# Kernel tuning notes

Measured on AMD Instinct MI355X. Metric: run time of the kernel, lower is better.

## Reference

```python
import jax, jax.numpy as jnp
import numpy as np

N_HEADS = 8
N_LEVELS = 1
N_POINTS = 4
D_MODEL = 256
BATCH = 2
H0, W0 = 100, 150
LS = H0 * W0
LQ = 15000


def layer_norm(x, g, b, eps=1e-5):
    m = jnp.mean(x, -1, keepdims=True)
    v = jnp.var(x, -1, keepdims=True)
    return (x - m) * jax.lax.rsqrt(v + eps) * g + b


def bilinear_sample(v, Hl, Wl, loc):
    # v: [N, Hl*Wl, Hh, D] level features; loc in [0,1]: [N, Lq, Hh, P, 2] (x, y)
    Nb, _, Hh, D = v.shape
    Lq, P = loc.shape[1], loc.shape[3]
    x = loc[..., 0] * Wl - 0.5           # align_corners=False grid_sample convention
    y = loc[..., 1] * Hl - 0.5
    x0 = jnp.floor(x); y0 = jnp.floor(y)
    lx = (x - x0).transpose(0, 2, 1, 3)[..., None]   # [N,Hh,Lq,P,1]
    ly = (y - y0).transpose(0, 2, 1, 3)[..., None]
    x0i = x0.astype(jnp.int32); y0i = y0.astype(jnp.int32)
    vh = v.transpose(0, 2, 1, 3)                      # [N,Hh,Hl*Wl,D]

    def gather(xi, yi):
        valid = (xi >= 0) & (xi < Wl) & (yi >= 0) & (yi < Hl)   # zero padding
        idx = jnp.clip(yi, 0, Hl - 1) * Wl + jnp.clip(xi, 0, Wl - 1)
        idxf = idx.transpose(0, 2, 1, 3).reshape(Nb, Hh, Lq * P)
        g = jnp.take_along_axis(vh, idxf[..., None], axis=2).reshape(Nb, Hh, Lq, P, D)
        return g * valid.transpose(0, 2, 1, 3)[..., None]

    g00 = gather(x0i, y0i)
    g10 = gather(x0i + 1, y0i)
    g01 = gather(x0i, y0i + 1)
    g11 = gather(x0i + 1, y0i + 1)
    return (g00 * (1 - lx) * (1 - ly) + g10 * lx * (1 - ly)
            + g01 * (1 - lx) * ly + g11 * lx * ly)   # [N,Hh,Lq,P,D]


def ms_deform_attn(q, reference_points, src, shapes_np, starts_np, padding_mask,
                   W_val, b_val, W_off, b_off, W_attn, b_attn, W_out, b_out):
    Nb, Lq, C = q.shape
    Hh, D, L, P = N_HEADS, C // N_HEADS, N_LEVELS, N_POINTS
    value = src @ W_val + b_val
    value = jnp.where(padding_mask[..., None], 0.0, value).reshape(Nb, -1, Hh, D)
    offsets = (q @ W_off + b_off).reshape(Nb, Lq, Hh, L, P, 2)
    aw = jax.nn.softmax((q @ W_attn + b_attn).reshape(Nb, Lq, Hh, L * P), -1)
    aw = aw.reshape(Nb, Lq, Hh, L, P)
    # offset normalizer is (W, H) per level
    norm = jnp.asarray(shapes_np[:, ::-1].copy(), dtype=q.dtype)   # [L,2]
    loc = reference_points[:, :, None, :, None, :] + offsets / norm[None, None, None, :, None, :]
    out = 0.0
    for l in range(L):
        Hl, Wl = int(shapes_np[l, 0]), int(shapes_np[l, 1])
        s = int(starts_np[l])
        sampled = bilinear_sample(value[:, s:s + Hl * Wl], Hl, Wl, loc[:, :, :, l])
        out = out + jnp.sum(sampled * aw[:, :, :, l].transpose(0, 2, 1, 3)[..., None], axis=3)
    out = out.transpose(0, 2, 1, 3).reshape(Nb, Lq, C)
    return out @ W_out + b_out


def reference(tgt, query_pos, src_pos, tgt_spatial_shapes, reference_points,
              depth_reference_points, src, src_spatial_shapes, frame_start_index,
              src_padding_mask,
              W_dsa, b_dsa, g_nds, b_nds, W_off, b_off, W_attn, b_attn,
              W_val, b_val, W_out, b_out, W_csa, b_csa, g_n1, b_n1,
              W_ff, b_ff, g_n3, b_n3):
    ss = np.asarray(src_spatial_shapes)      # static level shapes
    starts = np.asarray(frame_start_index)
    # depth scale adaptation
    src_a = layer_norm(src @ W_dsa + b_dsa, g_nds, b_nds)
    q = tgt + query_pos
    tgt2 = ms_deform_attn(q, reference_points, src_a, ss, starts, src_padding_mask,
                          W_val, b_val, W_off, b_off, W_attn, b_attn, W_out, b_out)
    tgt2 = tgt2 @ W_csa + b_csa
    t = layer_norm(tgt + tgt2, g_n1, b_n1)
    # FFN: single linear d_model->d_model with exact GELU (per source code)
    ff = jax.nn.gelu(t @ W_ff + b_ff, approximate=False)
    return layer_norm(t + ff, g_n3, b_n3)


def setup_inputs() -> dict:
    key = jax.random.key(0)
    ks = jax.random.split(key, 24)
    C = D_MODEL
    Hh, L, P = N_HEADS, N_LEVELS, N_POINTS

    def lin(k, fin, fout, scale=None):
        s = (1.0 / np.sqrt(fin)) if scale is None else scale
        return (jax.random.normal(k, (fin, fout), jnp.float32) * s).astype(jnp.float32)

    inp = {}
    inp['tgt'] = jax.random.normal(ks[0], (BATCH, LQ, C), jnp.float32)
    inp['query_pos'] = 0.1 * jax.random.normal(ks[1], (BATCH, LQ, C), jnp.float32)
    inp['src_pos'] = 0.1 * jax.random.normal(ks[2], (BATCH, LS, C), jnp.float32)
    inp['tgt_spatial_shapes'] = jnp.array([[H0, W0]], jnp.int32)
    inp['reference_points'] = jax.random.uniform(ks[3], (BATCH, LQ, L, 2), jnp.float32)
    inp['depth_reference_points'] = jax.random.uniform(ks[4], (BATCH, LQ, 1, 2), jnp.float32)
    inp['src'] = jax.random.normal(ks[5], (BATCH, LS, C), jnp.float32)
    inp['src_spatial_shapes'] = jnp.array([[H0, W0]], jnp.int32)
    inp['frame_start_index'] = jnp.array([0], jnp.int32)
    inp['src_padding_mask'] = jnp.zeros((BATCH, LS), jnp.bool_)
    # parameters
    inp['W_dsa'] = lin(ks[6], C, C); inp['b_dsa'] = jnp.zeros((C,), jnp.float32)
    inp['g_nds'] = jnp.ones((C,), jnp.float32); inp['b_nds'] = jnp.zeros((C,), jnp.float32)
    inp['W_off'] = lin(ks[7], C, Hh * L * P * 2, scale=0.01)
    inp['b_off'] = 0.5 * jax.random.normal(ks[8], (Hh * L * P * 2,), jnp.float32)
    inp['W_attn'] = lin(ks[9], C, Hh * L * P)
    inp['b_attn'] = jnp.zeros((Hh * L * P,), jnp.float32)
    inp['W_val'] = lin(ks[10], C, C); inp['b_val'] = jnp.zeros((C,), jnp.float32)
    inp['W_out'] = lin(ks[11], C, C); inp['b_out'] = jnp.zeros((C,), jnp.float32)
    inp['W_csa'] = lin(ks[12], C, C); inp['b_csa'] = jnp.zeros((C,), jnp.float32)
    inp['g_n1'] = jnp.ones((C,), jnp.float32); inp['b_n1'] = jnp.zeros((C,), jnp.float32)
    inp['W_ff'] = lin(ks[13], C, C); inp['b_ff'] = jnp.zeros((C,), jnp.float32)
    inp['g_n3'] = jnp.ones((C,), jnp.float32); inp['b_n3'] = jnp.zeros((C,), jnp.float32)
    return inp
```

## Files before the change

kernel.cpp:

```cpp
#include <hip/hip_runtime.h>
#include <hip/hip_bf16.h>
#include <math.h>

#define LQ   15000
#define LS_  15000
#define NB   2
#define ROWS (NB*LQ)
#define HGT  100
#define WID  150
#define KDIM 256

typedef __attribute__((ext_vector_type(8))) short bf16x8;
typedef __attribute__((ext_vector_type(4))) float f32x4;

enum { EP_BIAS_F32 = 0, EP_LN_BF = 1, EP_MASK_HM = 2, EP_RES_LN_BF = 3, EP_GELU_RES_LN_F32 = 4 };
enum { AM_BF16 = 0, AM_F32 = 1, AM_F32SUM = 2 };

__device__ inline short f2bf(float x) {
    __hip_bfloat16 h = __float2bfloat16(x);
    return *reinterpret_cast<short*>(&h);
}
__device__ inline unsigned pack2bf(float a, float b) {
    return ((unsigned)(unsigned short)f2bf(a)) | (((unsigned)(unsigned short)f2bf(b)) << 16);
}
__device__ inline float bf2f(short s) {
    return __uint_as_float(((unsigned)(unsigned short)s) << 16);
}
__device__ inline float gelu_exact(float x) {
    return 0.5f * x * (1.f + erff(x * 0.70710678118654752440f));
}

template<int NT, int EPI, int AMODE>
__global__ __launch_bounds__(256) void mfma_gemm(
    const void* __restrict__ Ap, const void* __restrict__ Ap2,
    const short* __restrict__ WT,
    const float* __restrict__ bias, void* __restrict__ Out,
    const void* __restrict__ Res, const unsigned char* __restrict__ mask,
    const float* __restrict__ lng, const float* __restrict__ lnb, int M)
{
    constexpr int BN = NT * 16;
    __shared__ short As[64][40];
    __shared__ short Bs[BN][40];
    __shared__ float sbias[BN], sg[BN], sb2[BN];

    const int tid  = threadIdx.x;
    const int bm0  = blockIdx.x * 64;
    const int wave = tid >> 6, lane = tid & 63;
    const int quad = lane >> 4, c = lane & 15;

    if (tid < BN) {
        sbias[tid] = bias ? bias[tid] : 0.f;
        if (EPI == EP_LN_BF || EPI == EP_RES_LN_BF || EPI == EP_GELU_RES_LN_F32) {
            sg[tid] = lng[tid]; sb2[tid] = lnb[tid];
        }
    }

    f32x4 acc[NT];
    #pragma unroll
    for (int t = 0; t < NT; ++t) acc[t] = (f32x4){0.f, 0.f, 0.f, 0.f};

    for (int k0 = 0; k0 < KDIM; k0 += 32) {
        if (AMODE != AM_BF16) {
            const float* A  = (const float*)Ap;
            const float* A2 = (const float*)Ap2;
            #pragma unroll
            for (int it = 0; it < 2; ++it) {
                int f = it * 256 + tid; int m = f >> 3; int ko = (f & 7) * 4;
                int r = bm0 + m; if (r > M - 1) r = M - 1;
                float4 v = *(const float4*)&A[(size_t)r * KDIM + k0 + ko];
                if (AMODE == AM_F32SUM) {
                    float4 w = *(const float4*)&A2[(size_t)r * KDIM + k0 + ko];
                    v.x += w.x; v.y += w.y; v.z += w.z; v.w += w.w;
                }
                int2 p; p.x = pack2bf(v.x, v.y); p.y = pack2bf(v.z, v.w);
                *(int2*)&As[m][ko] = p;
            }
        } else {
            const short* A = (const short*)Ap;
            int m = tid >> 2; int ko = (tid & 3) * 8;
            int r = bm0 + m; if (r > M - 1) r = M - 1;
            *(int4*)&As[m][ko] = *(const int4*)&A[(size_t)r * KDIM + k0 + ko];
        }
        #pragma unroll
        for (int it = 0; it < (BN * 4 + 255) / 256; ++it) {
            int f = it * 256 + tid;
            if (f < BN * 4) {
                int n = f >> 2; int ko = (f & 3) * 8;
                *(int4*)&Bs[n][ko] = *(const int4*)&WT[(size_t)n * KDIM + k0 + ko];
            }
        }
        __syncthreads();
        bf16x8 a = *(const bf16x8*)&As[wave * 16 + c][quad * 8];
        #pragma unroll
        for (int t = 0; t < NT; ++t) {
            bf16x8 b = *(const bf16x8*)&Bs[t * 16 + c][quad * 8];
            acc[t] = __builtin_amdgcn_mfma_f32_16x16x32_bf16(a, b, acc[t], 0, 0, 0);
        }
        __syncthreads();
    }

    const int r0 = bm0 + wave * 16 + quad * 4;
    if constexpr (EPI == EP_BIAS_F32) {
        float* O = (float*)Out;
        #pragma unroll
        for (int reg = 0; reg < 4; ++reg) {
            int r = r0 + reg;
            if (r < M) {
                #pragma unroll
                for (int t = 0; t < NT; ++t)
                    O[(size_t)r * BN + t * 16 + c] = acc[t][reg] + sbias[t * 16 + c];
            }
        }
    } else if constexpr (EPI == EP_MASK_HM) {
        short* O = (short*)Out;
        #pragma unroll
        for (int reg = 0; reg < 4; ++reg) {
            int r = r0 + reg;
            if (r < M) {
                float mz = mask[r] ? 0.f : 1.f;
                int n = (r >= LS_) ? 1 : 0;
                int s = r - n * LS_;
                #pragma unroll
                for (int t = 0; t < NT; ++t) {
                    int col = t * 16 + c;
                    int h = col >> 5, d = col & 31;
                    O[(((size_t)n * 8 + h) * LS_ + s) * 32 + d] =
                        f2bf((acc[t][reg] + sbias[col]) * mz);
                }
            }
        }
    } else {
        #pragma unroll
        for (int reg = 0; reg < 4; ++reg) {
            int r = r0 + reg;
            int rl = (r < M) ? r : (M - 1);
            float s = 0.f, sq = 0.f;
            #pragma unroll
            for (int t = 0; t < NT; ++t) {
                float v = acc[t][reg] + sbias[t * 16 + c];
                if constexpr (EPI == EP_GELU_RES_LN_F32) {
                    v = gelu_exact(v);
                    v += bf2f(((const short*)Res)[(size_t)rl * 256 + t * 16 + c]);
                } else if constexpr (EPI == EP_RES_LN_BF) {
                    v += ((const float*)Res)[(size_t)rl * 256 + t * 16 + c];
                }
                acc[t][reg] = v;
                s += v; sq += v * v;
            }
            #pragma unroll
            for (int o = 1; o < 16; o <<= 1) {
                s  += __shfl_xor(s,  o, 64);
                sq += __shfl_xor(sq, o, 64);
            }
            float mean = s * (1.f / 256.f);
            float var  = sq * (1.f / 256.f) - mean * mean;
            float rs   = rsqrtf(var + 1e-5f);
            if (r < M) {
                #pragma unroll
                for (int t = 0; t < NT; ++t) {
                    float o = (acc[t][reg] - mean) * rs * sg[t * 16 + c] + sb2[t * 16 + c];
                    if constexpr (EPI == EP_GELU_RES_LN_F32)
                        ((float*)Out)[(size_t)r * 256 + t * 16 + c] = o;
                    else
                        ((short*)Out)[(size_t)r * 256 + t * 16 + c] = f2bf(o);
                }
            }
        }
    }
}

__global__ __launch_bounds__(256) void transp_cvt(const float* __restrict__ W, short* __restrict__ WT)
{
    __shared__ float tile[64][65];
    int bx = blockIdx.x * 64, by = blockIdx.y * 64;
    int tid = threadIdx.x;
    #pragma unroll
    for (int it = 0; it < 4; ++it) {
        int f = it * 256 + tid; int i = f >> 4; int j = (f & 15) * 4;
        float4 v = *(const float4*)&W[(size_t)(by + i) * 256 + bx + j];
        tile[i][j] = v.x; tile[i][j + 1] = v.y; tile[i][j + 2] = v.z; tile[i][j + 3] = v.w;
    }
    __syncthreads();
    #pragma unroll
    for (int it = 0; it < 16; ++it) {
        int f = it * 256 + tid; int nl = f >> 6; int kl = f & 63;
        WT[(size_t)(bx + nl) * 256 + by + kl] = f2bf(tile[kl][nl]);
    }
}

__global__ __launch_bounds__(256) void wc_kernel(
    const float* __restrict__ W_out, const float* __restrict__ W_csa, short* __restrict__ WT_c)
{
    int k = blockIdx.x, n = threadIdx.x;
    float s = 0.f;
    for (int j = 0; j < 256; ++j)
        s = fmaf(W_out[(size_t)k * 256 + j], W_csa[(size_t)j * 256 + n], s);
    WT_c[(size_t)n * 256 + k] = f2bf(s);
}

__global__ __launch_bounds__(256) void bias_combine_kernel(
    const float* __restrict__ b_out, const float* __restrict__ W_csa,
    const float* __restrict__ b_csa, float* __restrict__ bc)
{
    int j = threadIdx.x;
    float s = b_csa[j];
    for (int k = 0; k < 256; ++k) s = fmaf(b_out[k], W_csa[(size_t)k * 256 + j], s);
    bc[j] = s;
}

__global__ __launch_bounds__(256) void pack_oa(
    const float* __restrict__ W_off, const float* __restrict__ W_attn,
    const float* __restrict__ b_off, const float* __restrict__ b_attn,
    short* __restrict__ WT_oa, float* __restrict__ b_oa)
{
    int j = blockIdx.x, k = threadIdx.x;
    float v = (j < 64) ? W_off[(size_t)k * 64 + j] : W_attn[(size_t)k * 32 + (j - 64)];
    WT_oa[(size_t)j * 256 + k] = f2bf(v);
    if (k == 0) b_oa[j] = (j < 64) ? b_off[j] : b_attn[j - 64];
}

__global__ __launch_bounds__(256) void deform_sample(
    const short* __restrict__ value,
    const float* __restrict__ S_oa,
    const float* __restrict__ refp,
    short* __restrict__ out)
{
    int grp = blockIdx.x * 32 + (threadIdx.x >> 3);
    int c4  = threadIdx.x & 7;
    int h = grp & 7;
    int r = grp >> 3;
    int n = (r >= LS_) ? 1 : 0;

    const float* row = S_oa + (size_t)r * 96;
    float rx = refp[(size_t)r * 2 + 0], ry = refp[(size_t)r * 2 + 1];
    float4 oA = *(const float4*)&row[h * 8];
    float4 oB = *(const float4*)&row[h * 8 + 4];
    float4 lg = *(const float4*)&row[64 + h * 4];

    float mx = fmaxf(fmaxf(lg.x, lg.y), fmaxf(lg.z, lg.w));
    float e0 = expf(lg.x - mx), e1 = expf(lg.y - mx), e2 = expf(lg.z - mx), e3 = expf(lg.w - mx);
    float inv = 1.f / (e0 + e1 + e2 + e3);
    float aw[4] = {e0 * inv, e1 * inv, e2 * inv, e3 * inv};
    float ox[4] = {oA.x, oA.z, oB.x, oB.z};
    float oy[4] = {oA.y, oA.w, oB.y, oB.w};

    const short* vb = value + (((size_t)n * 8 + h) * LS_) * 32 + c4 * 4;
    float a0 = 0.f, a1 = 0.f, a2 = 0.f, a3 = 0.f;

    #pragma unroll
    for (int p = 0; p < 4; ++p) {
        float x = rx * (float)WID + ox[p] - 0.5f;
        float y = ry * (float)HGT + oy[p] - 0.5f;
        float x0f = floorf(x), y0f = floorf(y);
        float lx = x - x0f, ly = y - y0f;
        int x0 = (int)x0f, y0 = (int)y0f;
        int x1 = x0 + 1, y1 = y0 + 1;
        bool vx0 = (x0 >= 0) & (x0 < WID), vx1 = (x1 >= 0) & (x1 < WID);
        bool vy0 = (y0 >= 0) & (y0 < HGT), vy1 = (y1 >= 0) & (y1 < HGT);
        float w00 = (vx0 & vy0) ? (1.f - lx) * (1.f - ly) * aw[p] : 0.f;
        float w10 = (vx1 & vy0) ? lx * (1.f - ly) * aw[p] : 0.f;
        float w01 = (vx0 & vy1) ? (1.f - lx) * ly * aw[p] : 0.f;
        float w11 = (vx1 & vy1) ? lx * ly * aw[p] : 0.f;
        int xc0 = min(max(x0, 0), WID - 1), xc1 = min(max(x1, 0), WID - 1);
        int yc0 = min(max(y0, 0), HGT - 1), yc1 = min(max(y1, 0), HGT - 1);
        int2 v00 = *(const int2*)&vb[(size_t)(yc0 * WID + xc0) * 32];
        int2 v10 = *(const int2*)&vb[(size_t)(yc0 * WID + xc1) * 32];
        int2 v01 = *(const int2*)&vb[(size_t)(yc1 * WID + xc0) * 32];
        int2 v11 = *(const int2*)&vb[(size_t)(yc1 * WID + xc1) * 32];
        a0 += w00 * __uint_as_float(((unsigned)v00.x) << 16)
            + w10 * __uint_as_float(((unsigned)v10.x) << 16)
            + w01 * __uint_as_float(((unsigned)v01.x) << 16)
            + w11 * __uint_as_float(((unsigned)v11.x) << 16);
        a1 += w00 * __uint_as_float(v00.x & 0xffff0000u)
            + w10 * __uint_as_float(v10.x & 0xffff0000u)
            + w01 * __uint_as_float(v01.x & 0xffff0000u)
            + w11 * __uint_as_float(v11.x & 0xffff0000u);
        a2 += w00 * __uint_as_float(((unsigned)v00.y) << 16)
            + w10 * __uint_as_float(((unsigned)v10.y) << 16)
            + w01 * __uint_as_float(((unsigned)v01.y) << 16)
            + w11 * __uint_as_float(((unsigned)v11.y) << 16);
        a3 += w00 * __uint_as_float(v00.y & 0xffff0000u)
            + w10 * __uint_as_float(v10.y & 0xffff0000u)
            + w01 * __uint_as_float(v01.y & 0xffff0000u)
            + w11 * __uint_as_float(v11.y & 0xffff0000u);
    }
    int2 o;
    o.x = pack2bf(a0, a1);
    o.y = pack2bf(a2, a3);
    *(int2*)&out[(size_t)r * 256 + h * 32 + c4 * 4] = o;
}

extern "C" void kernel_launch(void* const* d_in, const int* in_sizes, int n_in,
                              void* d_out, int out_size, void* d_ws, size_t ws_size,
                              hipStream_t stream)
{
    const float* tgt       = (const float*)d_in[0];
    const float* query_pos = (const float*)d_in[1];
    const float* refp      = (const float*)d_in[4];
    const float* src       = (const float*)d_in[6];
    const unsigned char* mask = (const unsigned char*)d_in[9];
    const float* W_dsa  = (const float*)d_in[10]; const float* b_dsa  = (const float*)d_in[11];
    const float* g_nds  = (const float*)d_in[12]; const float* b_nds  = (const float*)d_in[13];
    const float* W_off  = (const float*)d_in[14]; const float* b_off  = (const float*)d_in[15];
    const float* W_attn = (const float*)d_in[16]; const float* b_attn = (const float*)d_in[17];
    const float* W_val  = (const float*)d_in[18]; const float* b_val  = (const float*)d_in[19];
    const float* W_out  = (const float*)d_in[20]; const float* b_out  = (const float*)d_in[21];
    const float* W_csa  = (const float*)d_in[22]; const float* b_csa  = (const float*)d_in[23];
    const float* g_n1   = (const float*)d_in[24]; const float* b_n1   = (const float*)d_in[25];
    const float* W_ff   = (const float*)d_in[26]; const float* b_ff   = (const float*)d_in[27];
    const float* g_n3   = (const float*)d_in[28]; const float* b_n3   = (const float*)d_in[29];
    float* out = (float*)d_out;

    short* bf0   = (short*)d_ws;
    short* bf1   = bf0 + (size_t)ROWS * 256;
    short* bf2   = bf1 + (size_t)ROWS * 256;
    float* S_oa  = (float*)(bf2 + (size_t)ROWS * 256);
    short* WT_dsa = (short*)(S_oa + (size_t)ROWS * 96);
    short* WT_val = WT_dsa + 65536;
    short* WT_c   = WT_val + 65536;
    short* WT_ff  = WT_c + 65536;
    short* WT_oa  = WT_ff + 65536;
    float* bc     = (float*)(WT_oa + 96 * 256);
    float* b_oa   = bc + 256;

    dim3 blk(256);
    const int GB = (ROWS + 63) / 64;

    transp_cvt<<<dim3(4, 4), blk, 0, stream>>>(W_dsa, WT_dsa);
    transp_cvt<<<dim3(4, 4), blk, 0, stream>>>(W_val, WT_val);
    transp_cvt<<<dim3(4, 4), blk, 0, stream>>>(W_ff,  WT_ff);
    wc_kernel<<<256, blk, 0, stream>>>(W_out, W_csa, WT_c);
    bias_combine_kernel<<<1, blk, 0, stream>>>(b_out, W_csa, b_csa, bc);
    pack_oa<<<96, blk, 0, stream>>>(W_off, W_attn, b_off, b_attn, WT_oa, b_oa);

    mfma_gemm<16, EP_LN_BF, AM_F32><<<GB, blk, 0, stream>>>(
        src, nullptr, WT_dsa, b_dsa, bf0, nullptr, nullptr, g_nds, b_nds, ROWS);
    mfma_gemm<16, EP_MASK_HM, AM_BF16><<<GB, blk, 0, stream>>>(
        bf0, nullptr, WT_val, b_val, bf2, nullptr, mask, nullptr, nullptr, ROWS);
    mfma_gemm<6, EP_BIAS_F32, AM_F32SUM><<<GB, blk, 0, stream>>>(
        tgt, query_pos, WT_oa, b_oa, S_oa, nullptr, nullptr, nullptr, nullptr, ROWS);
    deform_sample<<<ROWS * 8 / 32, blk, 0, stream>>>(bf2, S_oa, refp, bf0);
    mfma_gemm<16, EP_RES_LN_BF, AM_BF16><<<GB, blk, 0, stream>>>(
        bf0, nullptr, WT_c, bc, bf1, tgt, nullptr, g_n1, b_n1, ROWS);
    mfma_gemm<16, EP_GELU_RES_LN_F32, AM_BF16><<<GB, blk, 0, stream>>>(
        bf1, nullptr, WT_ff, b_ff, out, bf1, nullptr, g_n3, b_n3, ROWS);
}
```

Baseline: 347.0 us.

## Use persistent GEMM with full weight matrix resident in LDS

New measurement: 700.0 us. 102% more time.

```diff
diff --git a/kernel.cpp b/kernel.cpp
--- a/kernel.cpp
+++ b/kernel.cpp
@@ -8,7 +8,6 @@
 #define ROWS (NB*LQ)
 #define HGT  100
 #define WID  150
-#define KDIM 256
 
 typedef __attribute__((ext_vector_type(8))) short bf16x8;
 typedef __attribute__((ext_vector_type(4))) float f32x4;
@@ -31,192 +30,140 @@
 }
 
 template<int NT, int EPI, int AMODE>
-__global__ __launch_bounds__(256) void mfma_gemm(
+__global__ __launch_bounds__(512, 2) void pgemm(
     const void* __restrict__ Ap, const void* __restrict__ Ap2,
-    const short* __restrict__ WT,
-    const float* __restrict__ bias, void* __restrict__ Out,
-    const void* __restrict__ Res, const unsigned char* __restrict__ mask,
+    const short* __restrict__ WT, const float* __restrict__ bias,
+    void* __restrict__ Out, const void* __restrict__ Res,
+    const unsigned char* __restrict__ mask,
     const float* __restrict__ lng, const float* __restrict__ lnb, int M)
 {
     constexpr int BN = NT * 16;
-    __shared__ short As[64][40];
-    __shared__ short Bs[BN][40];
-    __shared__ float sbias[BN], sg[BN], sb2[BN];
+    __shared__ short Bs[BN][264];
 
     const int tid  = threadIdx.x;
-    const int bm0  = blockIdx.x * 64;
     const int wave = tid >> 6, lane = tid & 63;
     const int quad = lane >> 4, c = lane & 15;
 
-    if (tid < BN) {
-        sbias[tid] = bias ? bias[tid] : 0.f;
-        if (EPI == EP_LN_BF || EPI == EP_RES_LN_BF || EPI == EP_GELU_RES_LN_F32) {
-            sg[tid] = lng[tid]; sb2[tid] = lnb[tid];
-        }
+    #pragma unroll
+    for (int id = tid; id < BN * 32; id += 512) {
+        int n = id >> 5, kc = id & 31;
+        *(int4*)&Bs[n][kc * 8] = *(const int4*)&WT[(size_t)n * 256 + kc * 8];
     }
-
-    f32x4 acc[NT];
-    #pragma unroll
-    for (int t = 0; t < NT; ++t) acc[t] = (f32x4){0.f, 0.f, 0.f, 0.f};
-
-    for (int k0 = 0; k0 < KDIM; k0 += 32) {
-        if (AMODE != AM_BF16) {
+    __syncthreads();
+
+    const int ntiles = (M + 15) >> 4;
+    for (int task = blockIdx.x * 8 + wave; task < ntiles; task += gridDim.x * 8) {
+        const int r0 = task * 16;
+        int ra = r0 + c; if (ra > M - 1) ra = M - 1;
+
+        bf16x8 a[8];
+        if (AMODE == AM_BF16) {
+            const short* A = (const short*)Ap;
+            #pragma unroll
+            for (int k = 0; k < 8; ++k)
+                a[k] = *(const bf16x8*)&A[(size_t)ra * 256 + k * 32 + quad * 8];
+        } else {
             const float* A  = (const float*)Ap;
             const float* A2 = (const float*)Ap2;
             #pragma unroll
-            for (int it = 0; it < 2; ++it) {
-                int f = it * 256 + tid; int m = f >> 3; int ko = (f & 7) * 4;
-                int r = bm0 + m; if (r > M - 1) r = M - 1;
-                float4 v = *(const float4*)&A[(size_t)r * KDIM + k0 + ko];
+            for (int k = 0; k < 8; ++k) {
+                size_t base = (size_t)ra * 256 + k * 32 + quad * 8;
+                float4 v0 = *(const float4*)&A[base];
+                float4 v1 = *(const float4*)&A[base + 4];
                 if (AMODE == AM_F32SUM) {
-                    float4 w = *(const float4*)&A2[(size_t)r * KDIM + k0 + ko];
-                    v.x += w.x; v.y += w.y; v.z += w.z; v.w += w.w;
-                }
-                int2 p; p.x = pack2bf(v.x, v.y); p.y = pack2bf(v.z, v.w);
-                *(int2*)&As[m][ko] = p;
+                    float4 w0 = *(const float4*)&A2[base];
+                    float4 w1 = *(const float4*)&A2[base + 4];
+                    v0.x += w0.x; v0.y += w0.y; v0.z += w0.z; v0.w += w0.w;
+                    v1.x += w1.x; v1.y += w1.y; v1.z += w1.z; v1.w += w1.w;
+                }
+                int4 p;
+                p.x = pack2bf(v0.x, v0.y); p.y = pack2bf(v0.z, v0.w);
+                p.z = pack2bf(v1.x, v1.y); p.w = pack2bf(v1.z, v1.w);
+                a[k] = *(bf16x8*)&p;
+            }
+        }
+
+        f32x4 acc[NT];
+        #pragma unroll
+        for (int t = 0; t < NT; ++t) acc[t] = (f32x4){0.f, 0.f, 0.f, 0.f};
+
+        #pragma unroll
+        for (int k = 0; k < 8; ++k) {
+            #pragma unroll
+            for (int t = 0; t < NT; ++t) {
+                bf16x8 b = *(const bf16x8*)&Bs[t * 16 + c][k * 32 + quad * 8];
+                acc[t] = __builtin_amdgcn_mfma_f32_16x16x32_bf16(a[k], b, acc[t], 0, 0, 0);
+            }
+        }
+
+        if constexpr (EPI == EP_BIAS_F32) {
+            float* O = (float*)Out;
+            #pragma unroll
+            for (int reg = 0; reg < 4; ++reg) {
+                int r = r0 + quad * 4 + reg;
+                if (r < M) {
+                    #pragma unroll
+                    for (int t = 0; t < NT; ++t) {
+                        int col = t * 16 + c;
+                        O[(size_t)r * BN + col] = acc[t][reg] + bias[col];
+                    }
+                }
+            }
+        } else if constexpr (EPI == EP_MASK_HM) {
+            short* O = (short*)Out;
+            #pragma unroll
+            for (int reg = 0; reg < 4; ++reg) {
+                int r = r0 + quad * 4 + reg;
+                if (r < M) {
+                    float mz = mask[r] ? 0.f : 1.f;
+                    int n = (r >= LS_) ? 1 : 0;
+                    int sidx = r - n * LS_;
+                    #pragma unroll
+                    for (int t = 0; t < NT; ++t) {
+                        int col = t * 16 + c; int h = col >> 5, d = col & 31;
+                        O[(((size_t)n * 8 + h) * LS_ + sidx) * 32 + d] =
+                            f2bf((acc[t][reg] + bias[col]) * mz);
+                    }
+                }
             }
         } else {
-            const short* A = (const short*)Ap;
-            int m = tid >> 2; int ko = (tid & 3) * 8;
-            int r = bm0 + m; if (r > M - 1) r = M - 1;
-            *(int4*)&As[m][ko] = *(const int4*)&A[(size_t)r * KDIM + k0 + ko];
-        }
-        #pragma unroll
-        for (int it = 0; it < (BN * 4 + 255) / 256; ++it) {
-            int f = it * 256 + tid;
-            if (f < BN * 4) {
-                int n = f >> 2; int ko = (f & 3) * 8;
-                *(int4*)&Bs[n][ko] = *(const int4*)&WT[(size_t)n * KDIM + k0 + ko];
-            }
-        }
-        __syncthreads();
-        bf16x8 a = *(const bf16x8*)&As[wave * 16 + c][quad * 8];
-        #pragma unroll
-        for (int t = 0; t < NT; ++t) {
-            bf16x8 b = *(const bf16x8*)&Bs[t * 16 + c][quad * 8];
-            acc[t] = __builtin_amdgcn_mfma_f32_16x16x32_bf16(a, b, acc[t], 0, 0, 0);
-        }
-        __syncthreads();
-    }
-
-    const int r0 = bm0 + wave * 16 + quad * 4;
-    if constexpr (EPI == EP_BIAS_F32) {
-        float* O = (float*)Out;
-        #pragma unroll
-        for (int reg = 0; reg < 4; ++reg) {
-            int r = r0 + reg;
-            if (r < M) {
-                #pragma unroll
-                for (int t = 0; t < NT; ++t)
-                    O[(size_t)r * BN + t * 16 + c] = acc[t][reg] + sbias[t * 16 + c];
-            }
-        }
-    } else if constexpr (EPI == EP_MASK_HM) {
-        short* O = (short*)Out;
-        #pragma unroll
-        for (int reg = 0; reg < 4; ++reg) {
-            int r = r0 + reg;
-            if (r < M) {
-                float mz = mask[r] ? 0.f : 1.f;
-                int n = (r >= LS_) ? 1 : 0;
-                int s = r - n * LS_;
+            #pragma unroll
+            for (int reg = 0; reg < 4; ++reg) {
+                int r = r0 + quad * 4 + reg;
+                int rl = (r < M) ? r : (M - 1);
+                float s = 0.f, sq = 0.f;
+                float vv[NT];
                 #pragma unroll
                 for (int t = 0; t < NT; ++t) {
                     int col = t * 16 + c;
-                    int h = col >> 5, d = col & 31;
-                    O[(((size_t)n * 8 + h) * LS_ + s) * 32 + d] =
-                        f2bf((acc[t][reg] + sbias[col]) * mz);
-                }
-            }
-        }
-    } else {
-        #pragma unroll
-        for (int reg = 0; reg < 4; ++reg) {
-            int r = r0 + reg;
-            int rl = (r < M) ? r : (M - 1);
-            float s = 0.f, sq = 0.f;
-            #pragma unroll
-            for (int t = 0; t < NT; ++t) {
-                float v = acc[t][reg] + sbias[t * 16 + c];
-                if constexpr (EPI == EP_GELU_RES_LN_F32) {
-                    v = gelu_exact(v);
-                    v += bf2f(((const short*)Res)[(size_t)rl * 256 + t * 16 + c]);
-                } else if constexpr (EPI == EP_RES_LN_BF) {
-                    v += ((const float*)Res)[(size_t)rl * 256 + t * 16 + c];
-                }
-                acc[t][reg] = v;
-                s += v; sq += v * v;
-            }
-            #pragma unroll
-            for (int o = 1; o < 16; o <<= 1) {
-                s  += __shfl_xor(s,  o, 64);
-                sq += __shfl_xor(sq, o, 64);
-            }
-            float mean = s * (1.f / 256.f);
-            float var  = sq * (1.f / 256.f) - mean * mean;
-            float rs   = rsqrtf(var + 1e-5f);
-            if (r < M) {
+                    float v = acc[t][reg] + bias[col];
+                    if constexpr (EPI == EP_RES_LN_BF)
+                        v += ((const float*)Res)[(size_t)rl * 256 + col];
+                    else if constexpr (EPI == EP_GELU_RES_LN_F32)
+                        v = gelu_exact(v) + bf2f(((const short*)Res)[(size_t)rl * 256 + col]);
+                    vv[t] = v; s += v; sq += v * v;
+                }
                 #pragma unroll
-                for (int t = 0; t < NT; ++t) {
-                    float o = (acc[t][reg] - mean) * rs * sg[t * 16 + c] + sb2[t * 16 + c];
-                    if constexpr (EPI == EP_GELU_RES_LN_F32)
-                        ((float*)Out)[(size_t)r * 256 + t * 16 + c] = o;
-                    else
-                        ((short*)Out)[(size_t)r * 256 + t * 16 + c] = f2bf(o);
+                for (int o = 1; o < 16; o <<= 1) {
+                    s += __shfl_xor(s, o, 64); sq += __shfl_xor(sq, o, 64);
+                }
+                float mean = s * (1.f / 256.f);
+                float var  = sq * (1.f / 256.f) - mean * mean;
+                float rs   = rsqrtf(var + 1e-5f);
+                if (r < M) {
+                    #pragma unroll
+                    for (int t = 0; t < NT; ++t) {
+                        int col = t * 16 + c;
+                        float o = (vv[t] - mean) * rs * lng[col] + lnb[col];
+                        if constexpr (EPI == EP_GELU_RES_LN_F32)
+                            ((float*)Out)[(size_t)r * 256 + col] = o;
+                        else
+                            ((short*)Out)[(size_t)r * 256 + col] = f2bf(o);
+                    }
                 }
             }
         }
     }
-}
-
-__global__ __launch_bounds__(256) void transp_cvt(const float* __restrict__ W, short* __restrict__ WT)
-{
-    __shared__ float tile[64][65];
-    int bx = blockIdx.x * 64, by = blockIdx.y * 64;
-    int tid = threadIdx.x;
-    #pragma unroll
-    for (int it = 0; it < 4; ++it) {
-        int f = it * 256 + tid; int i = f >> 4; int j = (f & 15) * 4;
-        float4 v = *(const float4*)&W[(size_t)(by + i) * 256 + bx + j];
-        tile[i][j] = v.x; tile[i][j + 1] = v.y; tile[i][j + 2] = v.z; tile[i][j + 3] = v.w;
-    }
-    __syncthreads();
-    #pragma unroll
-    for (int it = 0; it < 16; ++it) {
-        int f = it * 256 + tid; int nl = f >> 6; int kl = f & 63;
-        WT[(size_t)(bx + nl) * 256 + by + kl] = f2bf(tile[kl][nl]);
-    }
-}
-
-__global__ __launch_bounds__(256) void wc_kernel(
-    const float* __restrict__ W_out, const float* __restrict__ W_csa, short* __restrict__ WT_c)
-{
-    int k = blockIdx.x, n = threadIdx.x;
-    float s = 0.f;
-    for (int j = 0; j < 256; ++j)
-        s = fmaf(W_out[(size_t)k * 256 + j], W_csa[(size_t)j * 256 + n], s);
-    WT_c[(size_t)n * 256 + k] = f2bf(s);
-}
-
-__global__ __launch_bounds__(256) void bias_combine_kernel(
-    const float* __restrict__ b_out, const float* __restrict__ W_csa,
-    const float* __restrict__ b_csa, float* __restrict__ bc)
-{
-    int j = threadIdx.x;
-    float s = b_csa[j];
-    for (int k = 0; k < 256; ++k) s = fmaf(b_out[k], W_csa[(size_t)k * 256 + j], s);
-    bc[j] = s;
-}
-
-__global__ __launch_bounds__(256) void pack_oa(
-    const float* __restrict__ W_off, const float* __restrict__ W_attn,
-    const float* __restrict__ b_off, const float* __restrict__ b_attn,
-    short* __restrict__ WT_oa, float* __restrict__ b_oa)
-{
-    int j = blockIdx.x, k = threadIdx.x;
-    float v = (j < 64) ? W_off[(size_t)k * 64 + j] : W_attn[(size_t)k * 32 + (j - 64)];
-    WT_oa[(size_t)j * 256 + k] = f2bf(v);
-    if (k == 0) b_oa[j] = (j < 64) ? b_off[j] : b_attn[j - 64];
 }
 
 __global__ __launch_bounds__(256) void deform_sample(
@@ -290,6 +237,57 @@
     *(int2*)&out[(size_t)r * 256 + h * 32 + c4 * 4] = o;
 }
 
+__global__ __launch_bounds__(256) void prep_all(
+    const float* __restrict__ W_dsa, const float* __restrict__ W_val,
+    const float* __restrict__ W_ff,  const float* __restrict__ W_out,
+    const float* __restrict__ W_csa, const float* __restrict__ b_out,
+    const float* __restrict__ b_csa, const float* __restrict__ W_off,
+    const float* __restrict__ W_attn, const float* __restrict__ b_off,
+    const float* __restrict__ b_attn,
+    short* __restrict__ WT_dsa, short* __restrict__ WT_val, short* __restrict__ WT_ff,
+    short* __restrict__ WT_c, float* __restrict__ bc,
+    short* __restrict__ WT_oa, float* __restrict__ b_oa)
+{
+    __shared__ float tile[64][65];
+    const int b = blockIdx.x, tid = threadIdx.x;
+    if (b < 48) {
+        const float* W = (b < 16) ? W_dsa : (b < 32) ? W_val : W_ff;
+        short* WT = (b < 16) ? WT_dsa : (b < 32) ? WT_val : WT_ff;
+        int t = b & 15; int bx = (t & 3) * 64, by = (t >> 2) * 64;
+        #pragma unroll
+        for (int it = 0; it < 4; ++it) {
+            int f = it * 256 + tid; int i = f >> 4; int j = (f & 15) * 4;
+            float4 v = *(const float4*)&W[(size_t)(by + i) * 256 + bx + j];
+            tile[i][j] = v.x; tile[i][j + 1] = v.y; tile[i][j + 2] = v.z; tile[i][j + 3] = v.w;
+        }
+        __syncthreads();
+        #pragma unroll
+        for (int it = 0; it < 16; ++it) {
+            int f = it * 256 + tid; int nl = f >> 6; int kl = f & 63;
+            WT[(size_t)(bx + nl) * 256 + by + kl] = f2bf(tile[kl][nl]);
+        }
+    } else if (b < 304) {
+        int k = b - 48, n = tid;
+        float s = 0.f;
+        #pragma unroll 8
+        for (int j = 0; j < 256; ++j)
+            s = fmaf(W_out[(size_t)k * 256 + j], W_csa[(size_t)j * 256 + n], s);
+        WT_c[(size_t)n * 256 + k] = f2bf(s);
+    } else if (b == 304) {
+        int j = tid;
+        float s = b_csa[j];
+        #pragma unroll 8
+        for (int k = 0; k < 256; ++k)
+            s = fmaf(b_out[k], W_csa[(size_t)k * 256 + j], s);
+        bc[j] = s;
+    } else {
+        int j = b - 305, k = tid;
+        float v = (j < 64) ? W_off[(size_t)k * 64 + j] : W_attn[(size_t)k * 32 + (j - 64)];
+        WT_oa[(size_t)j * 256 + k] = f2bf(v);
+        if (k == 0) b_oa[j] = (j < 64) ? b_off[j] : b_attn[j - 64];
+    }
+}
+
 extern "C" void kernel_launch(void* const* d_in, const int* in_sizes, int n_in,
                               void* d_out, int out_size, void* d_ws, size_t ws_size,
                               hipStream_t stream)
@@ -311,37 +309,38 @@
     const float* g_n3   = (const float*)d_in[28]; const float* b_n3   = (const float*)d_in[29];
     float* out = (float*)d_out;
 
-    short* bf0   = (short*)d_ws;
-    short* bf1   = bf0 + (size_t)ROWS * 256;
-    short* bf2   = bf1 + (size_t)ROWS * 256;
-    float* S_oa  = (float*)(bf2 + (size_t)ROWS * 256);
-    short* WT_dsa = (short*)(S_oa + (size_t)ROWS * 96);
-    short* WT_val = WT_dsa + 65536;
-    short* WT_c   = WT_val + 65536;
-    short* WT_ff  = WT_c + 65536;
-    short* WT_oa  = WT_ff + 65536;
-    float* bc     = (float*)(WT_oa + 96 * 256);
-    float* b_oa   = bc + 256;
-
-    dim3 blk(256);
-    const int GB = (ROWS + 63) / 64;
-
-    transp_cvt<<<dim3(4, 4), blk, 0, stream>>>(W_dsa, WT_dsa);
-    transp_cvt<<<dim3(4, 4), blk, 0, stream>>>(W_val, WT_val);
-    transp_cvt<<<dim3(4, 4), blk, 0, stream>>>(W_ff,  WT_ff);
-    wc_kernel<<<256, blk, 0, stream>>>(W_out, W_csa, WT_c);
-    bias_combine_kernel<<<1, blk, 0, stream>>>(b_out, W_csa, b_csa, bc);
-    pack_oa<<<96, blk, 0, stream>>>(W_off, W_attn, b_off, b_attn, WT_oa, b_oa);
-
-    mfma_gemm<16, EP_LN_BF, AM_F32><<<GB, blk, 0, stream>>>(
-        src, nullptr, WT_dsa, b_dsa, bf0, nullptr, nullptr, g_nds, b_nds, ROWS);
-    mfma_gemm<16, EP_MASK_HM, AM_BF16><<<GB, blk, 0, stream>>>(
-        bf0, nullptr, WT_val, b_val, bf2, nullptr, mask, nullptr, nullptr, ROWS);
-    mfma_gemm<6, EP_BIAS_F32, AM_F32SUM><<<GB, blk, 0, stream>>>(
+    short* buf0     = (short*)d_ws;
+    short* attn_out = buf0 + (size_t)ROWS * 256;
+    short* value    = attn_out + (size_t)ROWS * 256;
+    float* S_oa     = (float*)(value + (size_t)ROWS * 256);
+    short* WT_dsa   = (short*)(S_oa + (size_t)ROWS * 96);
+    short* WT_val   = WT_dsa + 65536;
+    short* WT_ff    = WT_val + 65536;
+    short* WT_c     = WT_ff + 65536;
+    short* WT_oa    = WT_c + 65536;
+    float* bc       = (float*)(WT_oa + 96 * 256);
+    float* b_oa     = bc + 256;
+
+    prep_all<<<401, dim3(256), 0, stream>>>(
+        W_dsa, W_val, W_ff, W_out, W_csa, b_out, b_csa, W_off, W_attn, b_off, b_attn,
+        WT_dsa, WT_val, WT_ff, WT_c, bc, WT_oa, b_oa);
+
+    dim3 pb(512);
+
+    pgemm<6, EP_BIAS_F32, AM_F32SUM><<<256, pb, 0, stream>>>(
         tgt, query_pos, WT_oa, b_oa, S_oa, nullptr, nullptr, nullptr, nullptr, ROWS);
-    deform_sample<<<ROWS * 8 / 32, blk, 0, stream>>>(bf2, S_oa, refp, bf0);
-    mfma_gemm<16, EP_RES_LN_BF, AM_BF16><<<GB, blk, 0, stream>>>(
-        bf0, nullptr, WT_c, bc, bf1, tgt, nullptr, g_n1, b_n1, ROWS);
-    mfma_gemm<16, EP_GELU_RES_LN_F32, AM_BF16><<<GB, blk, 0, stream>>>(
-        bf1, nullptr, WT_ff, b_ff, out, bf1, nullptr, g_n3, b_n3, ROWS);
-}
+
+    pgemm<16, EP_LN_BF, AM_F32><<<256, pb, 0, stream>>>(
+        src, nullptr, WT_dsa, b_dsa, buf0, nullptr, nullptr, g_nds, b_nds, ROWS);
+
+    pgemm<16, EP_MASK_HM, AM_BF16><<<256, pb, 0, stream>>>(
+        buf0, nullptr, WT_val, b_val, value, nullptr, mask, nullptr, nullptr, ROWS);
+
+    deform_sample<<<ROWS * 8 / 32, dim3(256), 0, stream>>>(value, S_oa, refp, attn_out);
+
+    pgemm<16, EP_RES_LN_BF, AM_BF16><<<256, pb, 0, stream>>>(
+        attn_out, nullptr, WT_c, bc, buf0, tgt, nullptr, g_n1, b_n1, ROWS);
+
+    pgemm<16, EP_GELU_RES_LN_F32, AM_BF16><<<256, pb, 0, stream>>>(
+        buf0, nullptr, WT_ff, b_ff, out, buf0, nullptr, g_n3, b_n3, ROWS);
+}
```
